# Kernel tuning notes

Hardware: AMD Instinct MI355X
Metric: run time of the kernel (lower is better)

Reference implementation:

```python
import jax, jax.numpy as jnp
import numpy as np
import math

H, KVH, D = 15, 5, 64  # heads, kv heads, head_dim
ROPE_BASE = 10000.0
NEG = -1e9


def _rope_cos_sin(position_ids):
    # position_ids: [B, S] int -> cos/sin [B, 1, S, D]
    inv_freq = 1.0 / (ROPE_BASE ** (jnp.arange(0, D, 2, dtype=jnp.float32) / D))  # [D/2]
    freqs = position_ids.astype(jnp.float32)[..., None] * inv_freq  # [B, S, D/2]
    emb = jnp.concatenate([freqs, freqs], axis=-1)  # [B, S, D]
    return jnp.cos(emb)[:, None], jnp.sin(emb)[:, None]


def _rotate_half(x):
    x1, x2 = x[..., : D // 2], x[..., D // 2 :]
    return jnp.concatenate([-x2, x1], axis=-1)


def setup_inputs() -> dict:
    key = jax.random.key(0)
    ks = jax.random.split(key, 5)
    B, S, E = 1, 4096, 960
    hidden_states = jax.random.normal(ks[0], (B, S, E), dtype=jnp.float32)
    Wq = jax.random.normal(ks[1], (E, E), dtype=jnp.float32) * 0.02
    Wk = jax.random.normal(ks[2], (KVH * D, E), dtype=jnp.float32) * 0.02
    Wv = jax.random.normal(ks[3], (KVH * D, E), dtype=jnp.float32) * 0.02
    Wo = jax.random.normal(ks[4], (E, E), dtype=jnp.float32) * 0.02
    causal = jnp.tril(jnp.ones((S, S), dtype=bool))
    attention_mask = jnp.where(causal, 0.0, NEG).astype(jnp.float32)[None, None]  # [1,1,S,S]
    position_ids = jnp.arange(S, dtype=jnp.int64 if jax.config.jax_enable_x64 else jnp.int32)[None]
    return {
        "hidden_states": hidden_states,
        "Wq": Wq,
        "Wk": Wk,
        "Wv": Wv,
        "Wo": Wo,
        "attention_mask": attention_mask,
        "position_ids": position_ids,
    }


def reference(hidden_states, Wq, Wk, Wv, Wo, attention_mask, position_ids):
    B, S, E = hidden_states.shape
    groups = H // KVH
    # projections (bias-free Linear: x @ W.T)
    q = (hidden_states @ Wq.T).reshape(B, S, H, D).transpose(0, 2, 1, 3)      # [B,H,S,D]
    k = (hidden_states @ Wk.T).reshape(B, S, KVH, D).transpose(0, 2, 1, 3)    # [B,KVH,S,D]
    v = (hidden_states @ Wv.T).reshape(B, S, KVH, D).transpose(0, 2, 1, 3)    # [B,KVH,S,D]
    cos, sin = _rope_cos_sin(position_ids)  # [B,1,S,D]
    q = q * cos + _rotate_half(q) * sin
    k = k * cos + _rotate_half(k) * sin
    # GQA: repeat_interleave over the head axis
    k = jnp.repeat(k, groups, axis=1)  # [B,H,S,D]
    v = jnp.repeat(v, groups, axis=1)  # [B,H,S,D]
    scores = jnp.einsum("bhqd,bhkd->bhqk", q, k) / math.sqrt(D) + attention_mask
    probs = jax.nn.softmax(scores.astype(jnp.float32), axis=-1).astype(q.dtype)
    out = jnp.einsum("bhqk,bhkd->bhqd", probs, v)  # [B,H,S,D]
    out = out.transpose(0, 2, 1, 3).reshape(B, S, E)
    return out @ Wo.T
```

## Files before the change

kernel.cpp:

```cpp
#include <hip/hip_runtime.h>
#include <hip/hip_bf16.h>

typedef __hip_bfloat16 bf16;
typedef short bf16x8 __attribute__((ext_vector_type(8)));
typedef short bf16x4 __attribute__((ext_vector_type(4)));
typedef float f32x4 __attribute__((ext_vector_type(4)));

static constexpr int S_LEN = 4096;
static constexpr int EMB   = 960;
static constexpr int NH    = 15;
static constexpr int NKVH  = 5;
static constexpr int KV_E  = NKVH * 64;

__device__ __forceinline__ float scrub(float x, float lim) {
  return fminf(fmaxf(x, -lim), lim);
}

__device__ __forceinline__ short f2bf(float x) {
  bf16 h = __float2bfloat16(x);
  short s;
  __builtin_memcpy(&s, &h, 2);
  return s;
}

__device__ __forceinline__ void stage16(const bf16* g, bf16* l) {
  __builtin_amdgcn_global_load_lds(
      (const __attribute__((address_space(1))) void*)g,
      (__attribute__((address_space(3))) void*)l, 16, 0, 0);
}

__global__ void cvt5_kernel(const float* s0, const float* s1, const float* s2,
                            const float* s3, const float* s4,
                            bf16* d0, bf16* d1, bf16* d2, bf16* d3, bf16* d4,
                            int e0, int e1, int e2, int e3, int e4) {
  int i = blockIdx.x * blockDim.x + threadIdx.x;
  const float* s;
  bf16* d;
  int base;
  if (i < e0)      { s = s0; d = d0; base = 0;  }
  else if (i < e1) { s = s1; d = d1; base = e0; }
  else if (i < e2) { s = s2; d = d2; base = e1; }
  else if (i < e3) { s = s3; d = d3; base = e2; }
  else if (i < e4) { s = s4; d = d4; base = e3; }
  else return;
  int k = i - base;
  const float4* sp = (const float4*)s + (size_t)k * 2;
  float4 a = sp[0], b = sp[1];
  bf16x8 r;
  r[0] = f2bf(a.x); r[1] = f2bf(a.y); r[2] = f2bf(a.z); r[3] = f2bf(a.w);
  r[4] = f2bf(b.x); r[5] = f2bf(b.y); r[6] = f2bf(b.z); r[7] = f2bf(b.w);
  *(bf16x8*)((short*)d + (size_t)k * 8) = r;
}

__global__ void zero_kernel(float* __restrict__ p, int n4) {
  int i = blockIdx.x * blockDim.x + threadIdx.x;
  if (i < n4) ((float4*)p)[i] = (float4){0.f, 0.f, 0.f, 0.f};
}

template <typename EPI>
__device__ __forceinline__ void gemm_core(
    const bf16* __restrict__ A, const bf16* __restrict__ W,
    int m0, int n0, int K, bf16* At0, bf16* At1, bf16* Bt0, bf16* Bt1,
    EPI&& epilogue) {
  const int lane = threadIdx.x & 63;
  const int wave = threadIdx.x >> 6;
  const int quad = lane >> 4;
  const int c16  = lane & 15;
  const int wm = wave >> 1, wn = wave & 1;
  const int srow = lane >> 2;
  const int sch  = lane & 3;
  const int NIT  = K / 32;
  bf16* At[2] = {At0, At1};
  bf16* Bt[2] = {Bt0, Bt1};

  auto stage = [&](int b, int k0) {
#pragma unroll
    for (int t = 0; t < 2; t++) {
      int j = wave * 2 + t;
      stage16(A + (size_t)(m0 + j * 16 + srow) * K + k0 + sch * 8,
              At[b] + j * 512);
      stage16(W + (size_t)(n0 + j * 16 + srow) * K + k0 + sch * 8,
              Bt[b] + j * 512);
    }
  };

  f32x4 acc[4][4];
#pragma unroll
  for (int i = 0; i < 4; i++)
#pragma unroll
    for (int j = 0; j < 4; j++) acc[i][j] = (f32x4){0.f, 0.f, 0.f, 0.f};

  stage(0, 0);
  __syncthreads();

  for (int it = 0; it < NIT; ++it) {
    if (it + 1 < NIT) stage((it + 1) & 1, (it + 1) * 32);
    const char* ab = (const char*)At[it & 1];
    const char* bb = (const char*)Bt[it & 1];
    bf16x8 af[4], bfr[4];
#pragma unroll
    for (int i = 0; i < 4; i++)
      af[i] = *(const bf16x8*)(ab + (wm * 64 + i * 16 + c16) * 64 + quad * 16);
#pragma unroll
    for (int j = 0; j < 4; j++)
      bfr[j] = *(const bf16x8*)(bb + (wn * 64 + j * 16 + c16) * 64 + quad * 16);
#pragma unroll
    for (int i = 0; i < 4; i++)
#pragma unroll
      for (int j = 0; j < 4; j++)
        acc[i][j] = __builtin_amdgcn_mfma_f32_16x16x32_bf16(af[i], bfr[j],
                                                            acc[i][j], 0, 0, 0);
    __syncthreads();
  }
  epilogue(acc, m0, n0, wm, wn, quad, c16);
}

__global__ __launch_bounds__(256) void gemm_qkv_kernel(
    const bf16* __restrict__ A, const bf16* __restrict__ Wcat,
    bf16* __restrict__ Qb, bf16* __restrict__ Kbf, bf16* __restrict__ VTb,
    int M, int K) {
  __shared__ __align__(16) bf16 At[2][128 * 32];
  __shared__ __align__(16) bf16 Bt[2][128 * 32];
  const int m0 = blockIdx.x * 128;
  const int n0 = blockIdx.y * 128;
  gemm_core(A, Wcat, m0, n0, K, At[0], At[1], Bt[0], Bt[1],
            [&](f32x4 (&acc)[4][4], int m0_, int n0_, int wm, int wn,
                int quad, int c16) {
#pragma unroll
              for (int i = 0; i < 4; i++)
#pragma unroll
                for (int j = 0; j < 4; j++) {
                  int scol = n0_ + wn * 64 + j * 16;
                  if (scol >= 1600) continue;
                  int colg = scol + c16;
                  int row0 = m0_ + wm * 64 + i * 16 + quad * 4;
                  if (scol < 960) {
#pragma unroll
                    for (int r = 0; r < 4; r++)
                      Qb[(size_t)(row0 + r) * EMB + colg] =
                          __float2bfloat16(scrub(acc[i][j][r], 3e4f));
                  } else if (scol < 1280) {
#pragma unroll
                    for (int r = 0; r < 4; r++)
                      Kbf[(size_t)(row0 + r) * KV_E + (colg - 960)] =
                          __float2bfloat16(scrub(acc[i][j][r], 3e4f));
                  } else {
                    bf16x4 v;
#pragma unroll
                    for (int r = 0; r < 4; r++)
                      v[r] = f2bf(scrub(acc[i][j][r], 3e4f));
                    *(bf16x4*)((short*)VTb + (size_t)(colg - 1280) * S_LEN +
                               row0) = v;
                  }
                }
            });
}

__global__ __launch_bounds__(256) void gemm_out_kernel(
    const bf16* __restrict__ A, const bf16* __restrict__ W,
    float* __restrict__ C, int M, int N, int K) {
  __shared__ __align__(16) bf16 At[2][128 * 32];
  __shared__ __align__(16) bf16 Bt[2][128 * 32];
  const int m0 = blockIdx.x * 128;
  const int n0 = blockIdx.y * 128;
  gemm_core(A, W, m0, n0, K, At[0], At[1], Bt[0], Bt[1],
            [&](f32x4 (&acc)[4][4], int m0_, int n0_, int wm, int wn,
                int quad, int c16) {
#pragma unroll
              for (int i = 0; i < 4; i++)
#pragma unroll
                for (int j = 0; j < 4; j++) {
                  int scol = n0_ + wn * 64 + j * 16;
                  if (scol >= EMB) continue;
                  int col = scol + c16;
                  int row0 = m0_ + wm * 64 + i * 16 + quad * 4;
#pragma unroll
                  for (int r = 0; r < 4; r++)
                    C[(size_t)(row0 + r) * EMB + col] =
                        scrub(acc[i][j][r], 3e4f);
                }
            });
}

__global__ void rope2_kernel(bf16* __restrict__ Qb, bf16* __restrict__ Kb,
                             const int* __restrict__ pos_ids) {
  int tid = blockIdx.x * blockDim.x + threadIdx.x;
  if (tid >= S_LEN * (NH + NKVH) * 32) return;
  int d  = tid & 31;
  int hh = (tid >> 5) % (NH + NKVH);
  int s  = tid / ((NH + NKVH) * 32);
  bf16* buf;
  size_t idx;
  float scale;
  if (hh < NH) {
    buf = Qb; idx = (size_t)s * EMB + hh * 64 + d; scale = 0.125f;
  } else {
    buf = Kb; idx = (size_t)s * KV_E + (hh - NH) * 64 + d; scale = 1.0f;
  }
  float x = __bfloat162float(buf[idx]);
  float y = __bfloat162float(buf[idx + 32]);
  float f = (float)pos_ids[s] * expf((float)d * -0.28782313662425572f);
  float sf, cf;
  sincosf(f, &sf, &cf);
  buf[idx]      = __float2bfloat16(scrub((x * cf - y * sf) * scale, 3e4f));
  buf[idx + 32] = __float2bfloat16(scrub((y * cf + x * sf) * scale, 3e4f));
}

__global__ __launch_bounds__(256) void flash_kernel(
    const bf16* __restrict__ Q, const bf16* __restrict__ Kb,
    const bf16* __restrict__ VT, float* __restrict__ Oacc,
    float* __restrict__ Lacc) {
  __shared__ __align__(16) bf16 Kt[2][64 * 64];
  __shared__ __align__(16) bf16 Vt[2][64 * 64];
  __shared__ __align__(16) bf16 pT[4][16 * 72];

  const int xq = (int)(gridDim.x - 1) - (int)blockIdx.x;
  const int c  = blockIdx.z;
  if (c > (xq >> 4)) return;

  const int lane = threadIdx.x & 63;
  const int wv   = threadIdx.x >> 6;
  const int quad = lane >> 4;
  const int c16  = lane & 15;
  const int h    = blockIdx.y;
  const int kvh  = h / 3;
  const int qb   = xq * 64;
  const int qw   = qb + wv * 16;
  const int it0   = c * 16;
  const int itend = min(it0 + 16, xq + 1);

  const int rsub = lane >> 3;
  const int gch  = (lane & 7) ^ rsub;

  const bf16* qrow = Q + (size_t)(qw + c16) * EMB + h * 64 + quad * 8;
  const bf16x8 aq0 = *(const bf16x8*)qrow;
  const bf16x8 aq1 = *(const bf16x8*)(qrow + 32);

  bf16x8 onesf;
#pragma unroll
  for (int j = 0; j < 8; j++) onesf[j] = (short)0x3F80;

  f32x4 o[4];
#pragma unroll
  for (int n = 0; n < 4; n++) o[n] = (f32x4){0.f, 0.f, 0.f, 0.f};
  f32x4 os = (f32x4){0.f, 0.f, 0.f, 0.f};
  bf16* pz = &pT[wv][0];

  auto stage = [&](int b, int it) {
    const int kbase = it * 64;
#pragma unroll
    for (int t = 0; t < 2; t++) {
      int i = wv * 2 + t;
      int r = i * 8 + rsub;
      stage16(Kb + (size_t)(kbase + r) * KV_E + kvh * 64 + gch * 8,
              &Kt[b][i * 512]);
      stage16(VT + (size_t)(kvh * 64 + r) * S_LEN + kbase + gch * 8,
              &Vt[b][i * 512]);
    }
  };

  stage(0, it0);
  __syncthreads();

  for (int it = it0; it < itend; ++it) {
    if (it + 1 < itend) stage((it + 1) & 1, it + 1);

    const int kbase = it * 64;
    const char* kb = (const char*)&Kt[it & 1][0];
    const char* vb = (const char*)&Vt[it & 1][0];

#pragma unroll
    for (int cc = 0; cc < 4; cc++) {
      int r = cc * 16 + c16;
      int s0 = ((quad ^ (r & 7)) * 16);
      bf16x8 b0 = *(const bf16x8*)(kb + r * 128 + s0);
      bf16x8 b1 = *(const bf16x8*)(kb + r * 128 + (s0 ^ 64));
      f32x4 s = (f32x4){0.f, 0.f, 0.f, 0.f};
      s = __builtin_amdgcn_mfma_f32_16x16x32_bf16(aq0, b0, s, 0, 0, 0);
      s = __builtin_amdgcn_mfma_f32_16x16x32_bf16(aq1, b1, s, 0, 0, 0);
      if (it == xq) {
        const int col = kbase + cc * 16 + c16;
#pragma unroll
        for (int r4 = 0; r4 < 4; r4++) {
          int row = qw + quad * 4 + r4;
          float p = __expf(fminf(s[r4], 80.f));
          p = (col <= row) ? p : 0.f;
          pz[(quad * 4 + r4) * 72 + cc * 16 + c16] = __float2bfloat16(p);
        }
      } else {
#pragma unroll
        for (int r4 = 0; r4 < 4; r4++)
          pz[(quad * 4 + r4) * 72 + cc * 16 + c16] =
              __float2bfloat16(__expf(fminf(s[r4], 80.f)));
      }
    }
    asm volatile("s_waitcnt lgkmcnt(0)" ::: "memory");
    bf16x8 ap0 = *(const bf16x8*)((const char*)pz + c16 * 144 + quad * 16);
    bf16x8 ap1 = *(const bf16x8*)((const char*)pz + c16 * 144 + 64 + quad * 16);
    asm volatile("" ::: "memory");

#pragma unroll
    for (int n = 0; n < 4; n++) {
      int rd = n * 16 + c16;
      int o0 = ((quad ^ (rd & 7)) * 16);
      bf16x8 v0 = *(const bf16x8*)(vb + rd * 128 + o0);
      bf16x8 v1 = *(const bf16x8*)(vb + rd * 128 + (o0 ^ 64));
      o[n] = __builtin_amdgcn_mfma_f32_16x16x32_bf16(ap0, v0, o[n], 0, 0, 0);
      o[n] = __builtin_amdgcn_mfma_f32_16x16x32_bf16(ap1, v1, o[n], 0, 0, 0);
    }
    os = __builtin_amdgcn_mfma_f32_16x16x32_bf16(ap0, onesf, os, 0, 0, 0);
    os = __builtin_amdgcn_mfma_f32_16x16x32_bf16(ap1, onesf, os, 0, 0, 0);

    __syncthreads();
  }

#pragma unroll
  for (int n = 0; n < 4; n++)
#pragma unroll
    for (int r = 0; r < 4; r++) {
      int row = qw + quad * 4 + r;
      int col = h * 64 + n * 16 + c16;
      atomicAdd(&Oacc[(size_t)row * EMB + col], o[n][r]);
    }
  if (c16 == 0) {
#pragma unroll
    for (int r = 0; r < 4; r++)
      atomicAdd(&Lacc[(size_t)(qw + quad * 4 + r) * NH + h], os[r]);
  }
}

__global__ void normalize_kernel(const float* __restrict__ Oacc,
                                 const float* __restrict__ Lacc,
                                 bf16* __restrict__ O) {
  int i = blockIdx.x * blockDim.x + threadIdx.x;
  if (i >= S_LEN * (EMB / 4)) return;
  int row = i / (EMB / 4);
  int col = (i % (EMB / 4)) * 4;
  int h = col >> 6;
  float l = fmaxf(Lacc[(size_t)row * NH + h], 1e-20f);
  float4 v = *(const float4*)&Oacc[(size_t)row * EMB + col];
  bf16x4 r;
  r[0] = f2bf(scrub(v.x / l, 1e4f));
  r[1] = f2bf(scrub(v.y / l, 1e4f));
  r[2] = f2bf(scrub(v.z / l, 1e4f));
  r[3] = f2bf(scrub(v.w / l, 1e4f));
  *(bf16x4*)((short*)O + (size_t)row * EMB + col) = r;
}

extern "C" void kernel_launch(void* const* d_in, const int* in_sizes, int n_in,
                              void* d_out, int out_size, void* d_ws, size_t ws_size,
                              hipStream_t stream) {
  const float* hs = (const float*)d_in[0];
  const float* Wq = (const float*)d_in[1];
  const float* Wk = (const float*)d_in[2];
  const float* Wv = (const float*)d_in[3];
  const float* Wo = (const float*)d_in[4];
  const int* pos = (const int*)d_in[6];
  float* out = (float*)d_out;

  char* wsb = (char*)d_ws;
  float* Oacc = (float*)wsb;
  float* Lacc = Oacc + (size_t)S_LEN * EMB;
  size_t regA = ((size_t)S_LEN * EMB + (size_t)S_LEN * NH) * sizeof(float);
  bf16* hsb = (bf16*)wsb;
  bf16* Qb  = (bf16*)(wsb + regA);
  bf16* Kbf = Qb + (size_t)S_LEN * EMB;
  bf16* VTb = Kbf + (size_t)S_LEN * KV_E;
  bf16* Wqb = VTb + (size_t)S_LEN * KV_E;
  bf16* Wkb = Wqb + (size_t)EMB * EMB;
  bf16* Wvb = Wkb + (size_t)KV_E * EMB;
  bf16* Wob = Wqb + (size_t)1664 * EMB;

  {
    int e0 = (S_LEN * EMB) / 8;
    int e1 = e0 + (EMB * EMB) / 8;
    int e2 = e1 + (KV_E * EMB) / 8;
    int e3 = e2 + (KV_E * EMB) / 8;
    int e4 = e3 + (EMB * EMB) / 8;
    cvt5_kernel<<<(e4 + 255) / 256, 256, 0, stream>>>(
        hs, Wq, Wk, Wv, Wo, hsb, Wqb, Wkb, Wvb, Wob, e0, e1, e2, e3, e4);
  }

  gemm_qkv_kernel<<<dim3(S_LEN / 128, 13), 256, 0, stream>>>(
      hsb, Wqb, Qb, Kbf, VTb, S_LEN, EMB);

  {
    int n = S_LEN * (NH + NKVH) * 32;
    rope2_kernel<<<(n + 255) / 256, 256, 0, stream>>>(Qb, Kbf, pos);
  }

  {
    int n4 = (S_LEN * EMB + S_LEN * NH) / 4;
    zero_kernel<<<(n4 + 255) / 256, 256, 0, stream>>>(Oacc, n4);
  }
  flash_kernel<<<dim3(S_LEN / 64, NH, 4), 256, 0, stream>>>(Qb, Kbf, VTb,
                                                            Oacc, Lacc);
  {
    int n = S_LEN * (EMB / 4);
    normalize_kernel<<<(n + 255) / 256, 256, 0, stream>>>(Oacc, Lacc, Qb);
  }

  gemm_out_kernel<<<dim3(S_LEN / 128, 8), 256, 0, stream>>>(
      Qb, Wob, out, S_LEN, EMB, EMB);
}
```

Baseline: 295.9 us.

## Process two 64-row query groups per block to reuse staged K/V tiles

Each flash block now covers 128 query rows, split into two 16-row groups per wave, so every K/V tile staged into shared memory feeds twice the MFMA work. The grid along the query dimension is halved, and the causal iteration range and split-K chunking are recomputed for 128-row blocks. The P scratch tile loses its padding and uses an XOR swizzle to avoid bank conflicts, and launch bounds now request 4 blocks per CU. The cost is doubled accumulator registers per wave (possible occupancy or spill risk) and fewer, larger blocks, which may hurt load balance.

New measurement: 310.0 us. 4.8% more time.

```diff
diff --git a/kernel.cpp b/kernel.cpp
--- a/kernel.cpp
+++ b/kernel.cpp
@@ -206,17 +206,20 @@
   buf[idx + 32] = __float2bfloat16(scrub((y * cf + x * sf) * scale, 3e4f));
 }
 
-__global__ __launch_bounds__(256) void flash_kernel(
+__global__ __launch_bounds__(256, 4) void flash_kernel(
     const bf16* __restrict__ Q, const bf16* __restrict__ Kb,
     const bf16* __restrict__ VT, float* __restrict__ Oacc,
     float* __restrict__ Lacc) {
   __shared__ __align__(16) bf16 Kt[2][64 * 64];
   __shared__ __align__(16) bf16 Vt[2][64 * 64];
-  __shared__ __align__(16) bf16 pT[4][16 * 72];
-
-  const int xq = (int)(gridDim.x - 1) - (int)blockIdx.x;
-  const int c  = blockIdx.z;
-  if (c > (xq >> 4)) return;
+  __shared__ __align__(16) bf16 pT[4][16 * 64];
+
+  const int xq  = (int)(gridDim.x - 1) - (int)blockIdx.x;
+  const int c   = blockIdx.z;
+  const int nit = 2 * xq + 2;
+  const int it0 = c * 16;
+  if (it0 >= nit) return;
+  const int itend = min(it0 + 16, nit);
 
   const int lane = threadIdx.x & 63;
   const int wv   = threadIdx.x >> 6;
@@ -224,27 +227,33 @@
   const int c16  = lane & 15;
   const int h    = blockIdx.y;
   const int kvh  = h / 3;
-  const int qb   = xq * 64;
-  const int qw   = qb + wv * 16;
-  const int it0   = c * 16;
-  const int itend = min(it0 + 16, xq + 1);
+  const int qb   = xq * 128;
+  const int qw[2] = {qb + wv * 16, qb + 64 + wv * 16};
 
   const int rsub = lane >> 3;
   const int gch  = (lane & 7) ^ rsub;
 
-  const bf16* qrow = Q + (size_t)(qw + c16) * EMB + h * 64 + quad * 8;
-  const bf16x8 aq0 = *(const bf16x8*)qrow;
-  const bf16x8 aq1 = *(const bf16x8*)(qrow + 32);
+  bf16x8 aq[2][2];
+#pragma unroll
+  for (int g = 0; g < 2; g++) {
+    const bf16* qrow = Q + (size_t)(qw[g] + c16) * EMB + h * 64 + quad * 8;
+    aq[g][0] = *(const bf16x8*)qrow;
+    aq[g][1] = *(const bf16x8*)(qrow + 32);
+  }
 
   bf16x8 onesf;
 #pragma unroll
   for (int j = 0; j < 8; j++) onesf[j] = (short)0x3F80;
 
-  f32x4 o[4];
-#pragma unroll
-  for (int n = 0; n < 4; n++) o[n] = (f32x4){0.f, 0.f, 0.f, 0.f};
-  f32x4 os = (f32x4){0.f, 0.f, 0.f, 0.f};
-  bf16* pz = &pT[wv][0];
+  f32x4 o[2][4];
+#pragma unroll
+  for (int g = 0; g < 2; g++)
+#pragma unroll
+    for (int n = 0; n < 4; n++) o[g][n] = (f32x4){0.f, 0.f, 0.f, 0.f};
+  f32x4 os[2] = {(f32x4){0.f, 0.f, 0.f, 0.f}, (f32x4){0.f, 0.f, 0.f, 0.f}};
+
+  char* pz = (char*)&pT[wv][0];
+  const int swr = ((c16 & 7) ^ (c16 >> 3)) << 4;
 
   auto stage = [&](int b, int it) {
     const int kbase = it * 64;
@@ -270,62 +279,70 @@
     const char* vb = (const char*)&Vt[it & 1][0];
 
 #pragma unroll
-    for (int cc = 0; cc < 4; cc++) {
-      int r = cc * 16 + c16;
-      int s0 = ((quad ^ (r & 7)) * 16);
-      bf16x8 b0 = *(const bf16x8*)(kb + r * 128 + s0);
-      bf16x8 b1 = *(const bf16x8*)(kb + r * 128 + (s0 ^ 64));
-      f32x4 s = (f32x4){0.f, 0.f, 0.f, 0.f};
-      s = __builtin_amdgcn_mfma_f32_16x16x32_bf16(aq0, b0, s, 0, 0, 0);
-      s = __builtin_amdgcn_mfma_f32_16x16x32_bf16(aq1, b1, s, 0, 0, 0);
-      if (it == xq) {
-        const int col = kbase + cc * 16 + c16;
+    for (int g = 0; g < 2; g++) {
+      if (g == 0 && it == 2 * xq + 1) continue;
+      const bool masked = (it == 2 * xq + g);
+
+#pragma unroll
+      for (int cc = 0; cc < 4; cc++) {
+        int r = cc * 16 + c16;
+        int s0 = ((quad ^ (r & 7)) * 16);
+        bf16x8 b0 = *(const bf16x8*)(kb + r * 128 + s0);
+        bf16x8 b1 = *(const bf16x8*)(kb + r * 128 + (s0 ^ 64));
+        f32x4 s = (f32x4){0.f, 0.f, 0.f, 0.f};
+        s = __builtin_amdgcn_mfma_f32_16x16x32_bf16(aq[g][0], b0, s, 0, 0, 0);
+        s = __builtin_amdgcn_mfma_f32_16x16x32_bf16(aq[g][1], b1, s, 0, 0, 0);
 #pragma unroll
         for (int r4 = 0; r4 < 4; r4++) {
-          int row = qw + quad * 4 + r4;
+          int row = quad * 4 + r4;
           float p = __expf(fminf(s[r4], 80.f));
-          p = (col <= row) ? p : 0.f;
-          pz[(quad * 4 + r4) * 72 + cc * 16 + c16] = __float2bfloat16(p);
+          if (masked) {
+            int col = kbase + cc * 16 + c16;
+            p = (col <= qw[g] + row) ? p : 0.f;
+          }
+          int sw = (((row & 7) ^ (row >> 3)) << 4);
+          *(bf16*)(pz + row * 128 + ((cc * 32 + c16 * 2) ^ sw)) =
+              __float2bfloat16(p);
         }
-      } else {
-#pragma unroll
-        for (int r4 = 0; r4 < 4; r4++)
-          pz[(quad * 4 + r4) * 72 + cc * 16 + c16] =
-              __float2bfloat16(__expf(fminf(s[r4], 80.f)));
       }
+      asm volatile("s_waitcnt lgkmcnt(0)" ::: "memory");
+      bf16x8 ap0 = *(const bf16x8*)(pz + c16 * 128 + ((quad * 16) ^ swr));
+      bf16x8 ap1 = *(const bf16x8*)(pz + c16 * 128 + ((quad * 16 + 64) ^ swr));
+      asm volatile("" ::: "memory");
+
+#pragma unroll
+      for (int n = 0; n < 4; n++) {
+        int rd = n * 16 + c16;
+        int o0 = ((quad ^ (rd & 7)) * 16);
+        bf16x8 v0 = *(const bf16x8*)(vb + rd * 128 + o0);
+        bf16x8 v1 = *(const bf16x8*)(vb + rd * 128 + (o0 ^ 64));
+        o[g][n] =
+            __builtin_amdgcn_mfma_f32_16x16x32_bf16(ap0, v0, o[g][n], 0, 0, 0);
+        o[g][n] =
+            __builtin_amdgcn_mfma_f32_16x16x32_bf16(ap1, v1, o[g][n], 0, 0, 0);
+      }
+      os[g] = __builtin_amdgcn_mfma_f32_16x16x32_bf16(ap0, onesf, os[g], 0, 0, 0);
+      os[g] = __builtin_amdgcn_mfma_f32_16x16x32_bf16(ap1, onesf, os[g], 0, 0, 0);
     }
-    asm volatile("s_waitcnt lgkmcnt(0)" ::: "memory");
-    bf16x8 ap0 = *(const bf16x8*)((const char*)pz + c16 * 144 + quad * 16);
-    bf16x8 ap1 = *(const bf16x8*)((const char*)pz + c16 * 144 + 64 + quad * 16);
-    asm volatile("" ::: "memory");
-
-#pragma unroll
-    for (int n = 0; n < 4; n++) {
-      int rd = n * 16 + c16;
-      int o0 = ((quad ^ (rd & 7)) * 16);
-      bf16x8 v0 = *(const bf16x8*)(vb + rd * 128 + o0);
-      bf16x8 v1 = *(const bf16x8*)(vb + rd * 128 + (o0 ^ 64));
-      o[n] = __builtin_amdgcn_mfma_f32_16x16x32_bf16(ap0, v0, o[n], 0, 0, 0);
-      o[n] = __builtin_amdgcn_mfma_f32_16x16x32_bf16(ap1, v1, o[n], 0, 0, 0);
+
+    __syncthreads();
+  }
+
+#pragma unroll
+  for (int g = 0; g < 2; g++) {
+#pragma unroll
+    for (int n = 0; n < 4; n++)
+#pragma unroll
+      for (int r = 0; r < 4; r++) {
+        int row = qw[g] + quad * 4 + r;
+        int col = h * 64 + n * 16 + c16;
+        atomicAdd(&Oacc[(size_t)row * EMB + col], o[g][n][r]);
+      }
+    if (c16 == 0) {
+#pragma unroll
+      for (int r = 0; r < 4; r++)
+        atomicAdd(&Lacc[(size_t)(qw[g] + quad * 4 + r) * NH + h], os[g][r]);
     }
-    os = __builtin_amdgcn_mfma_f32_16x16x32_bf16(ap0, onesf, os, 0, 0, 0);
-    os = __builtin_amdgcn_mfma_f32_16x16x32_bf16(ap1, onesf, os, 0, 0, 0);
-
-    __syncthreads();
-  }
-
-#pragma unroll
-  for (int n = 0; n < 4; n++)
-#pragma unroll
-    for (int r = 0; r < 4; r++) {
-      int row = qw + quad * 4 + r;
-      int col = h * 64 + n * 16 + c16;
-      atomicAdd(&Oacc[(size_t)row * EMB + col], o[n][r]);
-    }
-  if (c16 == 0) {
-#pragma unroll
-    for (int r = 0; r < 4; r++)
-      atomicAdd(&Lacc[(size_t)(qw + quad * 4 + r) * NH + h], os[r]);
   }
 }
 
@@ -393,8 +410,8 @@
     int n4 = (S_LEN * EMB + S_LEN * NH) / 4;
     zero_kernel<<<(n4 + 255) / 256, 256, 0, stream>>>(Oacc, n4);
   }
-  flash_kernel<<<dim3(S_LEN / 64, NH, 4), 256, 0, stream>>>(Qb, Kbf, VTb,
-                                                            Oacc, Lacc);
+  flash_kernel<<<dim3(S_LEN / 128, NH, 4), 256, 0, stream>>>(Qb, Kbf, VTb,
+                                                             Oacc, Lacc);
   {
     int n = S_LEN * (EMB / 4);
     normalize_kernel<<<(n + 255) / 256, 256, 0, stream>>>(Oacc, Lacc, Qb);
```

## Load K/V fragments directly from global memory, drop LDS staging and barriers

Applied to the files above, without the earlier changes.

The flash kernel stops double-buffering K and V tiles through shared memory. Each wave now loads its MFMA operand fragments straight from global memory (relying on L1/L2 reuse), which removes the per-iteration __syncthreads. The P scratch buffer is shrunk to 64 columns with an XOR swizzle, and launch bounds request 5 blocks per SM for higher occupancy. In exchange, every wave re-reads the same K/V data from cache instead of sharing one staged copy, and the global loads have no software prefetch.

New measurement: 581.2 us. 96.4% more time.

```diff
diff --git a/kernel.cpp b/kernel.cpp
--- a/kernel.cpp
+++ b/kernel.cpp
@@ -206,13 +206,11 @@
   buf[idx + 32] = __float2bfloat16(scrub((y * cf + x * sf) * scale, 3e4f));
 }
 
-__global__ __launch_bounds__(256) void flash_kernel(
+__global__ __launch_bounds__(256, 5) void flash_kernel(
     const bf16* __restrict__ Q, const bf16* __restrict__ Kb,
     const bf16* __restrict__ VT, float* __restrict__ Oacc,
     float* __restrict__ Lacc) {
-  __shared__ __align__(16) bf16 Kt[2][64 * 64];
-  __shared__ __align__(16) bf16 Vt[2][64 * 64];
-  __shared__ __align__(16) bf16 pT[4][16 * 72];
+  __shared__ __align__(16) bf16 pT[4][16 * 64];
 
   const int xq = (int)(gridDim.x - 1) - (int)blockIdx.x;
   const int c  = blockIdx.z;
@@ -224,14 +222,12 @@
   const int c16  = lane & 15;
   const int h    = blockIdx.y;
   const int kvh  = h / 3;
+  const int kvh64 = kvh * 64;
   const int qb   = xq * 64;
   const int qw   = qb + wv * 16;
   const int it0   = c * 16;
   const int itend = min(it0 + 16, xq + 1);
 
-  const int rsub = lane >> 3;
-  const int gch  = (lane & 7) ^ rsub;
-
   const bf16* qrow = Q + (size_t)(qw + c16) * EMB + h * 64 + quad * 8;
   const bf16x8 aq0 = *(const bf16x8*)qrow;
   const bf16x8 aq1 = *(const bf16x8*)(qrow + 32);
@@ -244,74 +240,60 @@
 #pragma unroll
   for (int n = 0; n < 4; n++) o[n] = (f32x4){0.f, 0.f, 0.f, 0.f};
   f32x4 os = (f32x4){0.f, 0.f, 0.f, 0.f};
-  bf16* pz = &pT[wv][0];
-
-  auto stage = [&](int b, int it) {
+
+  char* pz = (char*)&pT[wv][0];
+  const int swr = ((c16 & 7) ^ (c16 >> 3)) << 4;
+
+  for (int it = it0; it < itend; ++it) {
     const int kbase = it * 64;
-#pragma unroll
-    for (int t = 0; t < 2; t++) {
-      int i = wv * 2 + t;
-      int r = i * 8 + rsub;
-      stage16(Kb + (size_t)(kbase + r) * KV_E + kvh * 64 + gch * 8,
-              &Kt[b][i * 512]);
-      stage16(VT + (size_t)(kvh * 64 + r) * S_LEN + kbase + gch * 8,
-              &Vt[b][i * 512]);
-    }
-  };
-
-  stage(0, it0);
-  __syncthreads();
-
-  for (int it = it0; it < itend; ++it) {
-    if (it + 1 < itend) stage((it + 1) & 1, it + 1);
-
-    const int kbase = it * 64;
-    const char* kb = (const char*)&Kt[it & 1][0];
-    const char* vb = (const char*)&Vt[it & 1][0];
+    const bool masked = (it == xq);
 
 #pragma unroll
     for (int cc = 0; cc < 4; cc++) {
       int r = cc * 16 + c16;
-      int s0 = ((quad ^ (r & 7)) * 16);
-      bf16x8 b0 = *(const bf16x8*)(kb + r * 128 + s0);
-      bf16x8 b1 = *(const bf16x8*)(kb + r * 128 + (s0 ^ 64));
+      const bf16* kp = Kb + (size_t)(kbase + r) * KV_E + kvh64 + quad * 8;
+      bf16x8 b0 = *(const bf16x8*)kp;
+      bf16x8 b1 = *(const bf16x8*)(kp + 32);
       f32x4 s = (f32x4){0.f, 0.f, 0.f, 0.f};
       s = __builtin_amdgcn_mfma_f32_16x16x32_bf16(aq0, b0, s, 0, 0, 0);
       s = __builtin_amdgcn_mfma_f32_16x16x32_bf16(aq1, b1, s, 0, 0, 0);
-      if (it == xq) {
-        const int col = kbase + cc * 16 + c16;
-#pragma unroll
-        for (int r4 = 0; r4 < 4; r4++) {
-          int row = qw + quad * 4 + r4;
-          float p = __expf(fminf(s[r4], 80.f));
-          p = (col <= row) ? p : 0.f;
-          pz[(quad * 4 + r4) * 72 + cc * 16 + c16] = __float2bfloat16(p);
+#pragma unroll
+      for (int r4 = 0; r4 < 4; r4++) {
+        int row = quad * 4 + r4;
+        float p = __expf(fminf(s[r4], 80.f));
+        if (masked) {
+          int col = kbase + cc * 16 + c16;
+          p = (col <= qw + row) ? p : 0.f;
         }
-      } else {
-#pragma unroll
-        for (int r4 = 0; r4 < 4; r4++)
-          pz[(quad * 4 + r4) * 72 + cc * 16 + c16] =
-              __float2bfloat16(__expf(fminf(s[r4], 80.f)));
+        int sw = (((row & 7) ^ (row >> 3)) << 4);
+        *(bf16*)(pz + row * 128 + ((cc * 32 + c16 * 2) ^ sw)) =
+            __float2bfloat16(p);
       }
     }
-    asm volatile("s_waitcnt lgkmcnt(0)" ::: "memory");
-    bf16x8 ap0 = *(const bf16x8*)((const char*)pz + c16 * 144 + quad * 16);
-    bf16x8 ap1 = *(const bf16x8*)((const char*)pz + c16 * 144 + 64 + quad * 16);
-    asm volatile("" ::: "memory");
-
+
+    bf16x8 vfr[4][2];
 #pragma unroll
     for (int n = 0; n < 4; n++) {
       int rd = n * 16 + c16;
-      int o0 = ((quad ^ (rd & 7)) * 16);
-      bf16x8 v0 = *(const bf16x8*)(vb + rd * 128 + o0);
-      bf16x8 v1 = *(const bf16x8*)(vb + rd * 128 + (o0 ^ 64));
-      o[n] = __builtin_amdgcn_mfma_f32_16x16x32_bf16(ap0, v0, o[n], 0, 0, 0);
-      o[n] = __builtin_amdgcn_mfma_f32_16x16x32_bf16(ap1, v1, o[n], 0, 0, 0);
+      const bf16* vp = VT + (size_t)(kvh64 + rd) * S_LEN + kbase + quad * 8;
+      vfr[n][0] = *(const bf16x8*)vp;
+      vfr[n][1] = *(const bf16x8*)(vp + 32);
+    }
+
+    asm volatile("s_waitcnt lgkmcnt(0)" ::: "memory");
+    bf16x8 ap0 = *(const bf16x8*)(pz + c16 * 128 + ((quad * 16) ^ swr));
+    bf16x8 ap1 = *(const bf16x8*)(pz + c16 * 128 + ((quad * 16 + 64) ^ swr));
+    asm volatile("" ::: "memory");
+
+#pragma unroll
+    for (int n = 0; n < 4; n++) {
+      o[n] = __builtin_amdgcn_mfma_f32_16x16x32_bf16(ap0, vfr[n][0], o[n],
+                                                     0, 0, 0);
+      o[n] = __builtin_amdgcn_mfma_f32_16x16x32_bf16(ap1, vfr[n][1], o[n],
+                                                     0, 0, 0);
     }
     os = __builtin_amdgcn_mfma_f32_16x16x32_bf16(ap0, onesf, os, 0, 0, 0);
     os = __builtin_amdgcn_mfma_f32_16x16x32_bf16(ap1, onesf, os, 0, 0, 0);
-
-    __syncthreads();
   }
 
 #pragma unroll
```

## Compute transposed scores so P stays in registers, dropping LDS round-trip

Applied to the files above, without the earlier changes.

The QK^T MFMA operands are swapped so each lane holds a column of S^T, which matches the B-operand layout of the 16x16x16 bf16 MFMA for the PV product. The probability tile therefore stays in registers instead of being written to and read back from per-wave shared memory. The row sum is now accumulated in scalar registers with lane shuffles rather than by extra MFMAs against a ones vector. The output is transposed through the freed K buffer before the atomic adds, and launch bounds now request 5 blocks per CU. The tradeoff is more, smaller MFMAs and narrower V reads from LDS, plus a possible register cap imposed by the occupancy hint.

After: 288.0 us. -2.7%, faster.

```diff
diff --git a/kernel.cpp b/kernel.cpp
--- a/kernel.cpp
+++ b/kernel.cpp
@@ -206,13 +206,12 @@
   buf[idx + 32] = __float2bfloat16(scrub((y * cf + x * sf) * scale, 3e4f));
 }
 
-__global__ __launch_bounds__(256) void flash_kernel(
+__global__ __launch_bounds__(256, 5) void flash_kernel(
     const bf16* __restrict__ Q, const bf16* __restrict__ Kb,
     const bf16* __restrict__ VT, float* __restrict__ Oacc,
     float* __restrict__ Lacc) {
   __shared__ __align__(16) bf16 Kt[2][64 * 64];
   __shared__ __align__(16) bf16 Vt[2][64 * 64];
-  __shared__ __align__(16) bf16 pT[4][16 * 72];
 
   const int xq = (int)(gridDim.x - 1) - (int)blockIdx.x;
   const int c  = blockIdx.z;
@@ -226,25 +225,25 @@
   const int kvh  = h / 3;
   const int qb   = xq * 64;
   const int qw   = qb + wv * 16;
+  const int qcol = qw + c16;
   const int it0   = c * 16;
   const int itend = min(it0 + 16, xq + 1);
 
   const int rsub = lane >> 3;
   const int gch  = (lane & 7) ^ rsub;
-
-  const bf16* qrow = Q + (size_t)(qw + c16) * EMB + h * 64 + quad * 8;
+  const int rm   = c16 & 7;
+  const int ko0  = (quad ^ rm) * 16;
+  const int qh   = quad >> 1;
+  const int vsub = (quad & 1) * 8;
+
+  const bf16* qrow = Q + (size_t)qcol * EMB + h * 64 + quad * 8;
   const bf16x8 aq0 = *(const bf16x8*)qrow;
   const bf16x8 aq1 = *(const bf16x8*)(qrow + 32);
 
-  bf16x8 onesf;
-#pragma unroll
-  for (int j = 0; j < 8; j++) onesf[j] = (short)0x3F80;
-
   f32x4 o[4];
 #pragma unroll
   for (int n = 0; n < 4; n++) o[n] = (f32x4){0.f, 0.f, 0.f, 0.f};
-  f32x4 os = (f32x4){0.f, 0.f, 0.f, 0.f};
-  bf16* pz = &pT[wv][0];
+  float osum = 0.f;
 
   auto stage = [&](int b, int it) {
     const int kbase = it * 64;
@@ -268,64 +267,61 @@
     const int kbase = it * 64;
     const char* kb = (const char*)&Kt[it & 1][0];
     const char* vb = (const char*)&Vt[it & 1][0];
-
+    const bool masked = (it == xq);
+
+    bf16x4 pp[4];
 #pragma unroll
     for (int cc = 0; cc < 4; cc++) {
       int r = cc * 16 + c16;
-      int s0 = ((quad ^ (r & 7)) * 16);
-      bf16x8 b0 = *(const bf16x8*)(kb + r * 128 + s0);
-      bf16x8 b1 = *(const bf16x8*)(kb + r * 128 + (s0 ^ 64));
+      bf16x8 b0 = *(const bf16x8*)(kb + r * 128 + ko0);
+      bf16x8 b1 = *(const bf16x8*)(kb + r * 128 + (ko0 ^ 64));
       f32x4 s = (f32x4){0.f, 0.f, 0.f, 0.f};
-      s = __builtin_amdgcn_mfma_f32_16x16x32_bf16(aq0, b0, s, 0, 0, 0);
-      s = __builtin_amdgcn_mfma_f32_16x16x32_bf16(aq1, b1, s, 0, 0, 0);
-      if (it == xq) {
-        const int col = kbase + cc * 16 + c16;
-#pragma unroll
-        for (int r4 = 0; r4 < 4; r4++) {
-          int row = qw + quad * 4 + r4;
-          float p = __expf(fminf(s[r4], 80.f));
-          p = (col <= row) ? p : 0.f;
-          pz[(quad * 4 + r4) * 72 + cc * 16 + c16] = __float2bfloat16(p);
+      s = __builtin_amdgcn_mfma_f32_16x16x32_bf16(b0, aq0, s, 0, 0, 0);
+      s = __builtin_amdgcn_mfma_f32_16x16x32_bf16(b1, aq1, s, 0, 0, 0);
+#pragma unroll
+      for (int r4 = 0; r4 < 4; r4++) {
+        float p = __expf(fminf(s[r4], 80.f));
+        if (masked) {
+          int kc = kbase + cc * 16 + quad * 4 + r4;
+          p = (kc <= qcol) ? p : 0.f;
         }
-      } else {
-#pragma unroll
-        for (int r4 = 0; r4 < 4; r4++)
-          pz[(quad * 4 + r4) * 72 + cc * 16 + c16] =
-              __float2bfloat16(__expf(fminf(s[r4], 80.f)));
+        osum += p;
+        pp[cc][r4] = f2bf(p);
       }
     }
+
+#pragma unroll
+    for (int n = 0; n < 4; n++) {
+      const char* vrow = vb + (n * 16 + c16) * 128;
+#pragma unroll
+      for (int cc = 0; cc < 4; cc++) {
+        bf16x4 va =
+            *(const bf16x4*)(vrow + (((cc * 2 + qh) ^ rm) * 16) + vsub);
+        o[n] = __builtin_amdgcn_mfma_f32_16x16x16bf16_1k(va, pp[cc], o[n],
+                                                         0, 0, 0);
+      }
+    }
+
+    __syncthreads();
+  }
+
+  osum += __shfl_xor(osum, 16);
+  osum += __shfl_xor(osum, 32);
+  if (lane < 16)
+    atomicAdd(&Lacc[(size_t)(qw + lane) * NH + h], osum);
+
+  float* zone = (float*)((char*)&Kt[0][0] + wv * 1280 * 4);
+#pragma unroll
+  for (int n = 0; n < 4; n++) {
+    *(f32x4*)(zone + c16 * 20 + quad * 4) = o[n];
     asm volatile("s_waitcnt lgkmcnt(0)" ::: "memory");
-    bf16x8 ap0 = *(const bf16x8*)((const char*)pz + c16 * 144 + quad * 16);
-    bf16x8 ap1 = *(const bf16x8*)((const char*)pz + c16 * 144 + 64 + quad * 16);
+#pragma unroll
+    for (int r = 0; r < 4; r++) {
+      float t = zone[(quad * 4 + r) * 20 + c16];
+      atomicAdd(&Oacc[(size_t)(qw + quad * 4 + r) * EMB + h * 64 + n * 16 +
+                      c16], t);
+    }
     asm volatile("" ::: "memory");
-
-#pragma unroll
-    for (int n = 0; n < 4; n++) {
-      int rd = n * 16 + c16;
-      int o0 = ((quad ^ (rd & 7)) * 16);
-      bf16x8 v0 = *(const bf16x8*)(vb + rd * 128 + o0);
-      bf16x8 v1 = *(const bf16x8*)(vb + rd * 128 + (o0 ^ 64));
-      o[n] = __builtin_amdgcn_mfma_f32_16x16x32_bf16(ap0, v0, o[n], 0, 0, 0);
-      o[n] = __builtin_amdgcn_mfma_f32_16x16x32_bf16(ap1, v1, o[n], 0, 0, 0);
-    }
-    os = __builtin_amdgcn_mfma_f32_16x16x32_bf16(ap0, onesf, os, 0, 0, 0);
-    os = __builtin_amdgcn_mfma_f32_16x16x32_bf16(ap1, onesf, os, 0, 0, 0);
-
-    __syncthreads();
-  }
-
-#pragma unroll
-  for (int n = 0; n < 4; n++)
-#pragma unroll
-    for (int r = 0; r < 4; r++) {
-      int row = qw + quad * 4 + r;
-      int col = h * 64 + n * 16 + c16;
-      atomicAdd(&Oacc[(size_t)row * EMB + col], o[n][r]);
-    }
-  if (c16 == 0) {
-#pragma unroll
-    for (int r = 0; r < 4; r++)
-      atomicAdd(&Lacc[(size_t)(qw + quad * 4 + r) * NH + h], os[r]);
   }
 }
 
```
